# Performance work log

Measured on AMD Instinct MI355X. Metric: run time of the kernel, lower is better.

## Reference

```python
import jax, jax.numpy as jnp
import numpy as np

B, T, C = 8, 2048, 1024   # batch, seq_len, n_embd
H = 128                   # head_size

def setup_inputs() -> dict:
    key = jax.random.key(0)
    kx, kk, kq, kv = jax.random.split(key, 4)
    scale = 1.0 / np.sqrt(C)
    return {
        "x": jax.random.normal(kx, (B, T, C), dtype=jnp.float32),
        "Wk": jax.random.normal(kk, (C, H), dtype=jnp.float32) * scale,
        "Wq": jax.random.normal(kq, (C, H), dtype=jnp.float32) * scale,
        "Wv": jax.random.normal(kv, (C, H), dtype=jnp.float32) * scale,
    }

def reference(x, Wk, Wq, Wv):
    # k,q,v: [B,T,H]
    k = x @ Wk
    q = x @ Wq
    v = x @ Wv
    # NOTE: original scales by C**-0.5 (n_embd), not head_size**-0.5
    wei = jnp.einsum("bth,bsh->bts", q, k) * (x.shape[-1] ** -0.5)  # [B,T,T]
    wei = jax.nn.softmax(wei, axis=-1)  # no causal mask in the source module
    # dropout = 0.0 -> identity
    out = jnp.einsum("bts,bsh->bth", wei, v)  # [B,T,H]
    return out
```

## Files before the change

### kernel.cpp

```cpp
#include <hip/hip_runtime.h>
#include <hip/hip_bf16.h>
#include <stdint.h>
#include <stddef.h>

#define NB 8
#define NT 2048
#define NC 1024
#define NH 128

typedef float f32x4 __attribute__((ext_vector_type(4)));
typedef short bf16x8 __attribute__((ext_vector_type(8)));

__device__ __forceinline__ unsigned short f2bf(float f) {
    union { float f; uint32_t u; } v; v.f = f;
    uint32_t u = v.u;
    u += 0x7fffu + ((u >> 16) & 1u);
    return (unsigned short)(u >> 16);
}

__device__ __forceinline__ void gld16(const void* gp, void* lp) {
    __builtin_amdgcn_global_load_lds(
        (const __attribute__((address_space(1))) unsigned int*)gp,
        (__attribute__((address_space(3))) unsigned int*)lp, 16, 0, 0);
}


__global__ __launch_bounds__(256) void cast_w_kernel(const float* __restrict__ Wq,
                                                     const float* __restrict__ Wk,
                                                     const float* __restrict__ Wv,
                                                     unsigned short* __restrict__ Wtf) {
    int gid  = blockIdx.x * 256 + threadIdx.x;
    int lane = gid & 63;
    int fs   = gid >> 6;
    int kb   = fs & 31;
    int g    = fs >> 5;
    int w    = g >> 3;
    int g16  = g & 7;
    int quad = lane >> 4;
    int l16  = lane & 15;
    const float* src = (w == 0) ? Wq : ((w == 1) ? Wk : Wv);
    int n = g16 * 16 + l16;
    bf16x8 o;
#pragma unroll
    for (int j = 0; j < 8; ++j)
        o[j] = (short)f2bf(src[(size_t)(kb * 32 + quad * 8 + j) * 128 + n]);
    *(bf16x8*)(Wtf + (size_t)gid * 8) = o;
}

#define CS2 392

__global__ __launch_bounds__(256, 2) void proj_kernel(const float* __restrict__ x,
                                                      const unsigned short* __restrict__ Wtf,
                                                      unsigned short* __restrict__ Qf,
                                                      unsigned short* __restrict__ Kf,
                                                      unsigned short* __restrict__ Vf) {
    __shared__ __align__(16) unsigned short wbuf[2][24 * 512];

    const int tid  = threadIdx.x;
    const int wave = tid >> 6;
    const int lane = tid & 63;
    const int quad = lane >> 4;
    const int l16  = lane & 15;
    const int bidx = blockIdx.x;
    const int rowbase = bidx * 32;
    const int b    = bidx >> 6;
    const int mt   = wave & 1;
    const int nh   = wave >> 1;

    const float* xrow = x + (size_t)(rowbase + mt * 16 + l16) * NC;

    auto stageW = [&](int kb, int bi) {
#pragma unroll
        for (int i = 0; i < 6; ++i) {
            const int g = wave * 6 + i;
            gld16(Wtf + ((size_t)(g * 32 + kb) * 512) + lane * 8, &wbuf[bi][g * 512]);
        }
    };

    stageW(0, 0);
    __syncthreads();

    f32x4 acc[12] = {};
    for (int kb = 0; kb < 32; ++kb) {
        const int cur = kb & 1;
        if (kb < 31) stageW(kb + 1, cur ^ 1);
        const float* src = xrow + kb * 32 + quad * 8;
        float4 f0 = *(const float4*)src;
        float4 f1 = *(const float4*)(src + 4);
        bf16x8 a;
        a[0] = (short)f2bf(f0.x); a[1] = (short)f2bf(f0.y);
        a[2] = (short)f2bf(f0.z); a[3] = (short)f2bf(f0.w);
        a[4] = (short)f2bf(f1.x); a[5] = (short)f2bf(f1.y);
        a[6] = (short)f2bf(f1.z); a[7] = (short)f2bf(f1.w);
#pragma unroll
        for (int i = 0; i < 12; ++i) {
            bf16x8 wf = *(const bf16x8*)(&wbuf[cur][(nh * 12 + i) * 512 + lane * 8]);
            acc[i] = __builtin_amdgcn_mfma_f32_16x16x32_bf16(a, wf, acc[i], 0, 0, 0);
        }
        __syncthreads();
    }

    unsigned short* cs = (unsigned short*)wbuf;
#pragma unroll
    for (int i = 0; i < 12; ++i) {
        const int g = nh * 12 + i;
#pragma unroll
        for (int r = 0; r < 4; ++r)
            cs[(mt * 16 + quad * 4 + r) * CS2 + g * 16 + l16] = f2bf(acc[i][r]);
    }
    __syncthreads();

    const int ibase = (rowbase & (NT - 1)) >> 4;
    const int tc    = (rowbase & (NT - 1)) >> 5;
    unsigned short* qdst = Qf + (size_t)b * (NT * NH);
    unsigned short* kdst = Kf + (size_t)b * (NT * NH);
    unsigned short* vdst = Vf + (size_t)b * (NT * NH);

    {
        const int mq   = wave & 1;
        const int isK  = wave >> 1;
        unsigned short* dst = isK ? kdst : qdst;
        const int off = isK * 128;
        const int iqt = ibase + mq;
#pragma unroll
        for (int ks = 0; ks < 4; ++ks) {
            bf16x8 v = *(const bf16x8*)(&cs[(mq * 16 + l16) * CS2 + off + ks * 32 + quad * 8]);
            *(bf16x8*)(dst + ((size_t)(iqt * 4 + ks) * 64 + lane) * 8) = v;
        }
    }
#pragma unroll
    for (int i = 0; i < 2; ++i) {
        const int nt = wave * 2 + i;
        bf16x8 v;
#pragma unroll
        for (int j = 0; j < 8; ++j)
            v[j] = (short)cs[(quad * 8 + j) * CS2 + 256 + nt * 16 + l16];
        *(bf16x8*)(vdst + ((size_t)(nt * 64 + tc) * 64 + lane) * 8) = v;
    }
}

__global__ __launch_bounds__(256, 2) void attn_kernel(const unsigned short* __restrict__ Qf,
                                                      const unsigned short* __restrict__ Kf,
                                                      const unsigned short* __restrict__ Vf,
                                                      float* __restrict__ out) {
    __shared__ __align__(16) unsigned short kbuf[2][16 * 512];
    __shared__ __align__(16) unsigned short vbuf[2][16 * 512];
    __shared__ __align__(16) unsigned short p_all[4][16 * 40];
    __shared__ float sl[4][16];

    const int tid  = threadIdx.x;
    const int wave = tid >> 6;
    const int lane = tid & 63;
    const int quad = lane >> 4;
    const int l16  = lane & 15;
    const int bid  = blockIdx.x;
    const int b    = bid & 7;
    const int iqb  = bid >> 3;
    const int mt   = wave & 1;
    const int kh   = wave >> 1;
    const int iq   = iqb * 2 + mt;

    const unsigned short* qfp = Qf + (size_t)b * (NT * NH);
    const unsigned short* kfp = Kf + (size_t)b * (NT * NH);
    const unsigned short* vfp = Vf + (size_t)b * (NT * NH);
    unsigned short* p_w = p_all[wave];

    bf16x8 qf[4];
#pragma unroll
    for (int ks = 0; ks < 4; ++ks)
        qf[ks] = *(const bf16x8*)(qfp + ((size_t)(iq * 4 + ks) * 64 + lane) * 8);

    auto stage = [&](int j, int bi) {
#pragma unroll
        for (int i = 0; i < 8; ++i) {
            const int fid = wave * 8 + i;
            if (fid < 16) {
                gld16(kfp + ((size_t)(j * 16 + fid) * 512) + lane * 8, &kbuf[bi][fid * 512]);
            } else {
                const int s  = fid - 16;
                const int nt = s >> 1;
                const int c  = s & 1;
                gld16(vfp + ((size_t)(nt * 64 + j * 2 + c) * 512) + lane * 8, &vbuf[bi][s * 512]);
            }
        }
    };

    stage(0, 0);
    __syncthreads();

    f32x4 O[8] = {};
    float lsum[4] = {0.f, 0.f, 0.f, 0.f};
    const float scl2 = 0.03125f * 1.44269504088896340736f;

    for (int j = 0; j < 32; ++j) {
        const int cur = j & 1;
        if (j < 31) stage(j + 1, cur ^ 1);

        f32x4 S[2] = {};
#pragma unroll
        for (int ks = 0; ks < 4; ++ks) {
            bf16x8 kf0 = *(const bf16x8*)(&kbuf[cur][((kh * 2 + 0) * 4 + ks) * 512 + lane * 8]);
            bf16x8 kf1 = *(const bf16x8*)(&kbuf[cur][((kh * 2 + 1) * 4 + ks) * 512 + lane * 8]);
            S[0] = __builtin_amdgcn_mfma_f32_16x16x32_bf16(qf[ks], kf0, S[0], 0, 0, 0);
            S[1] = __builtin_amdgcn_mfma_f32_16x16x32_bf16(qf[ks], kf1, S[1], 0, 0, 0);
        }

#pragma unroll
        for (int n2 = 0; n2 < 2; ++n2) {
#pragma unroll
            for (int r = 0; r < 4; ++r) {
                float p = __builtin_amdgcn_exp2f(S[n2][r] * scl2);
                lsum[r] += p;
                p_w[(quad * 4 + r) * 40 + n2 * 16 + l16] = f2bf(p);
            }
        }

        bf16x8 pf = *(const bf16x8*)(&p_w[l16 * 40 + quad * 8]);
#pragma unroll
        for (int nt = 0; nt < 8; ++nt) {
            bf16x8 vf = *(const bf16x8*)(&vbuf[cur][(nt * 2 + kh) * 512 + lane * 8]);
            O[nt] = __builtin_amdgcn_mfma_f32_16x16x32_bf16(pf, vf, O[nt], 0, 0, 0);
        }

        __syncthreads();
    }

#pragma unroll
    for (int msk = 1; msk <= 8; msk <<= 1) {
#pragma unroll
        for (int r = 0; r < 4; ++r)
            lsum[r] += __shfl_xor(lsum[r], msk, 64);
    }

    if (l16 == 0) {
#pragma unroll
        for (int r = 0; r < 4; ++r)
            sl[wave][quad * 4 + r] = lsum[r];
    }
    float* so = (float*)kbuf;
    if (wave >= 2) {
#pragma unroll
        for (int nt = 0; nt < 8; ++nt) {
#pragma unroll
            for (int r = 0; r < 4; ++r)
                so[((size_t)(wave - 2) * 16 + quad * 4 + r) * 132 + nt * 16 + l16] = O[nt][r];
        }
    }
    __syncthreads();

    if (wave < 2) {
        float inv[4];
#pragma unroll
        for (int r = 0; r < 4; ++r)
            inv[r] = 1.0f / (sl[wave][quad * 4 + r] + sl[wave + 2][quad * 4 + r]);
        float* orow = out + ((size_t)b * NT + iq * 16) * NH;
#pragma unroll
        for (int nt = 0; nt < 8; ++nt) {
#pragma unroll
            for (int r = 0; r < 4; ++r) {
                float v = O[nt][r] + so[((size_t)wave * 16 + quad * 4 + r) * 132 + nt * 16 + l16];
                orow[(quad * 4 + r) * NH + nt * 16 + l16] = v * inv[r];
            }
        }
    }
}

extern "C" void kernel_launch(void* const* d_in, const int* in_sizes, int n_in,
                              void* d_out, int out_size, void* d_ws, size_t ws_size,
                              hipStream_t stream) {
    const float* x  = (const float*)d_in[0];
    const float* Wk = (const float*)d_in[1];
    const float* Wq = (const float*)d_in[2];
    const float* Wv = (const float*)d_in[3];
    float* out = (float*)d_out;

    char* ws = (char*)d_ws;
    unsigned short* Qf  = (unsigned short*)(ws);
    unsigned short* Kf  = (unsigned short*)(ws + 4194304);
    unsigned short* Vf  = (unsigned short*)(ws + 8388608);
    unsigned short* Wtf = (unsigned short*)(ws + 12582912);

    cast_w_kernel<<<192, 256, 0, stream>>>(Wq, Wk, Wv, Wtf);
    proj_kernel<<<512, 256, 0, stream>>>(x, Wtf, Qf, Kf, Vf);
    attn_kernel<<<512, 256, 0, stream>>>(Qf, Kf, Vf, out);
}
```

Measured before the change: 175.8 us.

## Restructure projection kernel to 64-row tiles with deeper W and x prefetch pipeline

The projection kernel now processes 64 rows per block with 512 threads (256 blocks), each wave computing two 16-row M tiles against 6 N tiles so every W fragment read from LDS feeds two MFMAs. W staging uses a 4-deep LDS ring buffer, and x loads are prefetched two k-steps ahead in registers. Synchronisation uses explicit vmcnt waits plus raw barriers instead of __syncthreads. The aim is to hide global load latency and halve W LDS traffic per FLOP, at the cost of more LDS (4x24KB) and register pressure, which could limit occupancy.

Result: no change. 177.1 us (+0.7%).

```diff
diff --git a/kernel.cpp b/kernel.cpp
--- a/kernel.cpp
+++ b/kernel.cpp
@@ -49,12 +49,12 @@
 
 #define CS2 392
 
-__global__ __launch_bounds__(256, 2) void proj_kernel(const float* __restrict__ x,
+__global__ __launch_bounds__(512, 2) void proj_kernel(const float* __restrict__ x,
                                                       const unsigned short* __restrict__ Wtf,
                                                       unsigned short* __restrict__ Qf,
                                                       unsigned short* __restrict__ Kf,
                                                       unsigned short* __restrict__ Vf) {
-    __shared__ __align__(16) unsigned short wbuf[2][24 * 512];
+    __shared__ __align__(16) unsigned short wbuf[4][24 * 512];
 
     const int tid  = threadIdx.x;
     const int wave = tid >> 6;
@@ -62,51 +62,77 @@
     const int quad = lane >> 4;
     const int l16  = lane & 15;
     const int bidx = blockIdx.x;
-    const int rowbase = bidx * 32;
-    const int b    = bidx >> 6;
-    const int mt   = wave & 1;
-    const int nh   = wave >> 1;
-
-    const float* xrow = x + (size_t)(rowbase + mt * 16 + l16) * NC;
-
-    auto stageW = [&](int kb, int bi) {
-#pragma unroll
-        for (int i = 0; i < 6; ++i) {
-            const int g = wave * 6 + i;
-            gld16(Wtf + ((size_t)(g * 32 + kb) * 512) + lane * 8, &wbuf[bi][g * 512]);
-        }
-    };
-
-    stageW(0, 0);
-    __syncthreads();
-
-    f32x4 acc[12] = {};
-    for (int kb = 0; kb < 32; ++kb) {
-        const int cur = kb & 1;
-        if (kb < 31) stageW(kb + 1, cur ^ 1);
-        const float* src = xrow + kb * 32 + quad * 8;
-        float4 f0 = *(const float4*)src;
-        float4 f1 = *(const float4*)(src + 4);
-        bf16x8 a;
-        a[0] = (short)f2bf(f0.x); a[1] = (short)f2bf(f0.y);
-        a[2] = (short)f2bf(f0.z); a[3] = (short)f2bf(f0.w);
-        a[4] = (short)f2bf(f1.x); a[5] = (short)f2bf(f1.y);
-        a[6] = (short)f2bf(f1.z); a[7] = (short)f2bf(f1.w);
-#pragma unroll
-        for (int i = 0; i < 12; ++i) {
-            bf16x8 wf = *(const bf16x8*)(&wbuf[cur][(nh * 12 + i) * 512 + lane * 8]);
-            acc[i] = __builtin_amdgcn_mfma_f32_16x16x32_bf16(a, wf, acc[i], 0, 0, 0);
-        }
-        __syncthreads();
-    }
+    const int rowbase = bidx * 64;
+    const int b    = bidx >> 5;
+    const int mh   = wave & 1;
+    const int nq   = wave >> 1;
+
+    const float* xr0 = x + (size_t)(rowbase + mh * 32 + l16) * NC;
+    const float* xr1 = xr0 + (size_t)16 * NC;
+
+    float4 aS[2][4];
+    f32x4 acc0[6] = {};
+    f32x4 acc1[6] = {};
+
+#define STAGE(KB, BI) { _Pragma("unroll") \
+    for (int i_ = 0; i_ < 3; ++i_) { \
+        const int g_ = wave * 3 + i_; \
+        gld16(Wtf + ((size_t)(g_ * 32 + (KB)) * 512) + lane * 8, &wbuf[BI][g_ * 512]); } }
+
+#define LOADA(KB, S) { \
+    const float* p0_ = xr0 + (KB) * 32 + quad * 8; \
+    aS[S][0] = *(const float4*)p0_; \
+    aS[S][1] = *(const float4*)(p0_ + 4); \
+    const float* p1_ = xr1 + (KB) * 32 + quad * 8; \
+    aS[S][2] = *(const float4*)p1_; \
+    aS[S][3] = *(const float4*)(p1_ + 4); }
+
+#define BARW(N) { asm volatile("s_waitcnt vmcnt(" #N ") lgkmcnt(0)" ::: "memory"); \
+                  __builtin_amdgcn_s_barrier(); }
+
+#define ITER(K, CUR, SLOT, DOA, DOST) { \
+    bf16x8 af0, af1; \
+    af0[0] = (short)f2bf(aS[SLOT][0].x); af0[1] = (short)f2bf(aS[SLOT][0].y); \
+    af0[2] = (short)f2bf(aS[SLOT][0].z); af0[3] = (short)f2bf(aS[SLOT][0].w); \
+    af0[4] = (short)f2bf(aS[SLOT][1].x); af0[5] = (short)f2bf(aS[SLOT][1].y); \
+    af0[6] = (short)f2bf(aS[SLOT][1].z); af0[7] = (short)f2bf(aS[SLOT][1].w); \
+    af1[0] = (short)f2bf(aS[SLOT][2].x); af1[1] = (short)f2bf(aS[SLOT][2].y); \
+    af1[2] = (short)f2bf(aS[SLOT][2].z); af1[3] = (short)f2bf(aS[SLOT][2].w); \
+    af1[4] = (short)f2bf(aS[SLOT][3].x); af1[5] = (short)f2bf(aS[SLOT][3].y); \
+    af1[6] = (short)f2bf(aS[SLOT][3].z); af1[7] = (short)f2bf(aS[SLOT][3].w); \
+    if (DOA)  LOADA((K) + 2, SLOT); \
+    if (DOST) STAGE((K) + 3, ((K) + 3) & 3); \
+    _Pragma("unroll") \
+    for (int i_ = 0; i_ < 6; ++i_) { \
+        bf16x8 wf_ = *(const bf16x8*)(&wbuf[CUR][(nq * 6 + i_) * 512 + lane * 8]); \
+        acc0[i_] = __builtin_amdgcn_mfma_f32_16x16x32_bf16(af0, wf_, acc0[i_], 0, 0, 0); \
+        acc1[i_] = __builtin_amdgcn_mfma_f32_16x16x32_bf16(af1, wf_, acc1[i_], 0, 0, 0); } }
+
+    LOADA(0, 0); LOADA(1, 1);
+    STAGE(0, 0); STAGE(1, 1); STAGE(2, 2);
+    BARW(6);
+
+    for (int kb4 = 0; kb4 < 28; kb4 += 4) {
+        ITER(kb4 + 0, 0, 0, 1, 1); BARW(14);
+        ITER(kb4 + 1, 1, 1, 1, 1); BARW(14);
+        ITER(kb4 + 2, 2, 0, 1, 1); BARW(14);
+        ITER(kb4 + 3, 3, 1, 1, 1); BARW(14);
+    }
+    ITER(28, 0, 0, 1, 1); BARW(14);
+    ITER(29, 1, 1, 1, 0); BARW(11);
+    ITER(30, 2, 0, 0, 0); BARW(4);
+    ITER(31, 3, 1, 0, 0);
+    asm volatile("s_waitcnt vmcnt(0) lgkmcnt(0)" ::: "memory");
+    __builtin_amdgcn_s_barrier();
 
     unsigned short* cs = (unsigned short*)wbuf;
 #pragma unroll
-    for (int i = 0; i < 12; ++i) {
-        const int g = nh * 12 + i;
-#pragma unroll
-        for (int r = 0; r < 4; ++r)
-            cs[(mt * 16 + quad * 4 + r) * CS2 + g * 16 + l16] = f2bf(acc[i][r]);
+    for (int i = 0; i < 6; ++i) {
+#pragma unroll
+        for (int r = 0; r < 4; ++r) {
+            cs[(mh * 32 +  0 + quad * 4 + r) * CS2 + nq * 96 + i * 16 + l16] = f2bf(acc0[i][r]);
+            cs[(mh * 32 + 16 + quad * 4 + r) * CS2 + nq * 96 + i * 16 + l16] = f2bf(acc1[i][r]);
+        }
     }
     __syncthreads();
 
@@ -116,27 +142,33 @@
     unsigned short* kdst = Kf + (size_t)b * (NT * NH);
     unsigned short* vdst = Vf + (size_t)b * (NT * NH);
 
-    {
-        const int mq   = wave & 1;
-        const int isK  = wave >> 1;
-        unsigned short* dst = isK ? kdst : qdst;
-        const int off = isK * 128;
-        const int iqt = ibase + mq;
-#pragma unroll
-        for (int ks = 0; ks < 4; ++ks) {
-            bf16x8 v = *(const bf16x8*)(&cs[(mq * 16 + l16) * CS2 + off + ks * 32 + quad * 8]);
-            *(bf16x8*)(dst + ((size_t)(iqt * 4 + ks) * 64 + lane) * 8) = v;
-        }
-    }
-#pragma unroll
-    for (int i = 0; i < 2; ++i) {
-        const int nt = wave * 2 + i;
-        bf16x8 v;
-#pragma unroll
-        for (int j = 0; j < 8; ++j)
-            v[j] = (short)cs[(quad * 8 + j) * CS2 + 256 + nt * 16 + l16];
-        *(bf16x8*)(vdst + ((size_t)(nt * 64 + tc) * 64 + lane) * 8) = v;
-    }
+#pragma unroll
+    for (int j = 0; j < 6; ++j) {
+        const int s = wave * 6 + j;
+        if (s < 32) {
+            const int isK = s >> 4;
+            const int t   = s & 15;
+            const int m   = t >> 2;
+            const int ks  = t & 3;
+            unsigned short* dst = isK ? kdst : qdst;
+            bf16x8 v = *(const bf16x8*)(&cs[(m * 16 + l16) * CS2 + isK * 128 + ks * 32 + quad * 8]);
+            *(bf16x8*)(dst + ((size_t)((ibase + m) * 4 + ks) * 64 + lane) * 8) = v;
+        } else {
+            const int vv = s - 32;
+            const int nt = vv >> 1;
+            const int cc = vv & 1;
+            bf16x8 v;
+#pragma unroll
+            for (int jj = 0; jj < 8; ++jj)
+                v[jj] = (short)cs[(cc * 32 + quad * 8 + jj) * CS2 + 256 + nt * 16 + l16];
+            *(bf16x8*)(vdst + ((size_t)(nt * 64 + tc + cc) * 64 + lane) * 8) = v;
+        }
+    }
+
+#undef ITER
+#undef BARW
+#undef LOADA
+#undef STAGE
 }
 
 __global__ __launch_bounds__(256, 2) void attn_kernel(const unsigned short* __restrict__ Qf,
@@ -281,6 +313,6 @@
     unsigned short* Wtf = (unsigned short*)(ws + 12582912);
 
     cast_w_kernel<<<192, 256, 0, stream>>>(Wq, Wk, Wv, Wtf);
-    proj_kernel<<<512, 256, 0, stream>>>(x, Wtf, Qf, Kf, Vf);
+    proj_kernel<<<256, 512, 0, stream>>>(x, Wtf, Qf, Kf, Vf);
     attn_kernel<<<512, 256, 0, stream>>>(Qf, Kf, Vf, out);
 }
```
